# Optimization experiments

Measured on AMD Instinct MI355X. Metric: run time of the kernel, lower is better.

## Reference

```python
import jax, jax.numpy as jnp
import numpy as np

B, C, H, W = 8, 64, 64, 64
DQK = C // 8  # q/k projection dim = 8


def setup_inputs() -> dict:
    key = jax.random.key(0)
    ks = jax.random.split(key, 5)
    return {
        "query": jax.random.normal(ks[0], (B, C, H, W), dtype=jnp.float32),
        "value": jax.random.normal(ks[1], (B, C, H, W), dtype=jnp.float32),
        "Wq": jax.random.normal(ks[2], (DQK, C), dtype=jnp.float32) * (1.0 / np.sqrt(C)),
        "bq": jnp.zeros((DQK,), dtype=jnp.float32),
        "Wk": jax.random.normal(ks[3], (DQK, C), dtype=jnp.float32) * (1.0 / np.sqrt(C)),
        "bk": jnp.zeros((DQK,), dtype=jnp.float32),
        "Wv": jax.random.normal(ks[4], (C, C), dtype=jnp.float32) * (1.0 / np.sqrt(C)),
        "bv": jnp.zeros((C,), dtype=jnp.float32),
    }


def reference(query, value, Wq, bq, Wk, bk, Wv, bv):
    b, c, h, w = value.shape
    n = h * w
    # 1x1 convs are per-pixel matmuls over channels
    q = jnp.einsum("oc,bchw->bohw", Wq, query) + bq[None, :, None, None]
    k = jnp.einsum("oc,bchw->bohw", Wk, query) + bk[None, :, None, None]
    v = jnp.einsum("oc,bchw->bohw", Wv, value) + bv[None, :, None, None]
    proj_q = q.reshape(b, DQK, n).transpose(0, 2, 1)  # [B, N, d]
    proj_k = k.reshape(b, DQK, n)                      # [B, d, N]
    energy = jnp.einsum("bnd,bdm->bnm", proj_q, proj_k)  # [B, N, N]
    attention = jax.nn.softmax(energy, axis=-1)
    proj_v = v.reshape(b, c, n)                        # [B, C, N]
    # out = proj_v @ attention^T
    out = jnp.einsum("bcm,bnm->bcn", proj_v, attention)
    out = out.reshape(b, c, h, w) + value
    return out
```

## Files before the change

### kernel.cpp

```cpp
#include <hip/hip_runtime.h>
#include <hip/hip_bf16.h>

typedef __attribute__((ext_vector_type(8))) __bf16 bf16x8;
typedef __attribute__((ext_vector_type(4))) float f32x4;

#if __has_builtin(__builtin_amdgcn_exp2f)
#define EXP2F(x) __builtin_amdgcn_exp2f(x)
#else
#define EXP2F(x) exp2f(x)
#endif

static constexpr int BB = 8, CC = 64, NN = 4096;
static constexpr size_t QF_OFF = 0;
static constexpr size_t KF_OFF = (size_t)2 << 20;
static constexpr size_t VF_OFF = (size_t)4 << 20;


__global__ __launch_bounds__(512) void proj_kernel(
    const float* __restrict__ query, const float* __restrict__ value,
    const float* __restrict__ Wq, const float* __restrict__ bq,
    const float* __restrict__ Wk, const float* __restrict__ bk,
    const float* __restrict__ Wv, const float* __restrict__ bv,
    char* __restrict__ ws) {
  __shared__ __bf16 vlds[64][72];
  __shared__ float  qlds[64][9];
  __shared__ float  klds[64][9];
  const float LOG2E = 1.4426950408889634f;
  int t = threadIdx.x;
  int part = __builtin_amdgcn_readfirstlane(t >> 6);
  int px = t & 63;
  int blk = blockIdx.x;
  int b = blk >> 6;
  int px0 = (blk & 63) << 6;
  size_t inbase = (size_t)b * CC * NN + px0 + px;

  bool isq = part < 4;
  int qko = (part & 3) * 2;
  const float* __restrict__ Wqk = isq ? Wq : Wk;

  float vacc[8];
  #pragma unroll
  for (int o = 0; o < 8; ++o) vacc[o] = bv[part * 8 + o];
  float qk0 = 0.f, qk1 = 0.f;

  #pragma unroll
  for (int cb = 0; cb < 4; ++cb) {
    float xq[16], xv[16];
    #pragma unroll
    for (int cc = 0; cc < 16; ++cc) {
      int c = cb * 16 + cc;
      xq[cc] = query[inbase + (size_t)c * NN];
      xv[cc] = value[inbase + (size_t)c * NN];
    }
    #pragma unroll
    for (int cc = 0; cc < 16; ++cc) {
      int c = cb * 16 + cc;
      qk0 += Wqk[qko * 64 + c] * xq[cc];
      qk1 += Wqk[(qko + 1) * 64 + c] * xq[cc];
      #pragma unroll
      for (int o = 0; o < 8; ++o) vacc[o] += Wv[(part * 8 + o) * 64 + c] * xv[cc];
    }
  }

  #pragma unroll
  for (int o = 0; o < 8; ++o) vlds[px][part * 8 + o] = (__bf16)vacc[o];
  if (isq) {
    qlds[px][qko]     = (qk0 + bq[qko]) * LOG2E;
    qlds[px][qko + 1] = (qk1 + bq[qko + 1]) * LOG2E;
  } else {
    klds[px][qko]     = qk0 + bk[qko];
    klds[px][qko + 1] = qk1 + bk[qko + 1];
  }
  __syncthreads();

  __bf16* qfrag = (__bf16*)(ws + QF_OFF);
  __bf16* kfrag = (__bf16*)(ws + KF_OFF);
  __bf16* vfrag = (__bf16*)(ws + VF_OFF);
  int l = t & 63, cp = l & 15, qd = l >> 4;

  {
    int jt = t >> 8, ct = (t >> 6) & 3;
    bf16x8 v8;
    #pragma unroll
    for (int r = 0; r < 8; ++r) {
      int jj = (r < 4) ? (4 * qd + r) : (16 + 4 * qd + (r & 3));
      v8[r] = vlds[jt * 32 + jj][ct * 16 + cp];
    }
    int jtg = (blk & 63) * 2 + jt;
    *(bf16x8*)(vfrag + ((((size_t)b * 128 + jtg) * 4 + ct) * 64 + l) * 8) = v8;
  }
  if (t < 256) {
    int jt = t >> 7, th = (t >> 6) & 1;
    int pxl = jt * 32 + th * 16 + (l & 15);
    bf16x8 k8;
    #pragma unroll
    for (int r = 0; r < 8; ++r) {
      float kv = klds[pxl][r];
      __bf16 hi = (__bf16)kv;
      __bf16 lo = (__bf16)(kv - (float)hi);
      k8[r] = (qd < 2) ? hi : lo;
    }
    int jtg = (blk & 63) * 2 + jt;
    *(bf16x8*)(kfrag + ((((size_t)b * 128 + jtg) * 2 + th) * 64 + l) * 8) = k8;
  } else {
    int it = (t >> 6) & 3;
    int il = it * 16 + (l & 15);
    bf16x8 q8;
    #pragma unroll
    for (int r = 0; r < 8; ++r) {
      float qv = qlds[il][r];
      __bf16 hi = (__bf16)qv;
      __bf16 lo = (__bf16)(qv - (float)hi);
      q8[r] = ((qd & 1) == 0) ? hi : lo;
    }
    int itg = (blk & 63) * 4 + it;
    *(bf16x8*)(qfrag + (((size_t)b * 256 + itg) * 64 + l) * 8) = q8;
  }
}

__global__ __launch_bounds__(512, 4) void attn_kernel(
    const char* __restrict__ ws, const float* __restrict__ value,
    float* __restrict__ out) {
  __shared__ float lds_acc[16 * 8 * 64];
  __shared__ float lds_l[4 * 8 * 64];
  const __bf16* qfrag = (const __bf16*)(ws + QF_OFF);
  const __bf16* kfrag = (const __bf16*)(ws + KF_OFF);
  const __bf16* vfrag = (const __bf16*)(ws + VF_OFF);
  int tid = threadIdx.x;
  int w = tid >> 6, lane = tid & 63;
  int blk = blockIdx.x;
  int b = blk >> 6;
  int i0 = (blk & 63) << 6;
  int itg0 = (blk & 63) * 4;

  bf16x8 qf[4];
  #pragma unroll
  for (int it = 0; it < 4; ++it)
    qf[it] = *(const bf16x8*)(qfrag + (((size_t)b * 256 + itg0 + it) * 64 + lane) * 8);

  f32x4 acc[4][4];
  #pragma unroll
  for (int ct = 0; ct < 4; ++ct)
    #pragma unroll
    for (int it = 0; it < 4; ++it) acc[ct][it] = (f32x4){0.f, 0.f, 0.f, 0.f};
  float lsum[4] = {0.f, 0.f, 0.f, 0.f};

  const __bf16* kb = kfrag + (((size_t)b * 128 + w * 16) * 2 * 64 + lane) * 8;
  const __bf16* vb = vfrag + (((size_t)b * 128 + w * 16) * 4 * 64 + lane) * 8;

  for (int itx = 0; itx < 16; ++itx) {
    bf16x8 kf0 = *(const bf16x8*)(kb);
    bf16x8 kf1 = *(const bf16x8*)(kb + 512);
    bf16x8 vf0 = *(const bf16x8*)(vb);
    bf16x8 vf1 = *(const bf16x8*)(vb + 512);
    bf16x8 vf2 = *(const bf16x8*)(vb + 1024);
    bf16x8 vf3 = *(const bf16x8*)(vb + 1536);
    const f32x4 z = (f32x4){0.f, 0.f, 0.f, 0.f};
    #pragma unroll
    for (int it = 0; it < 4; ++it) {
      f32x4 e0 = __builtin_amdgcn_mfma_f32_16x16x32_bf16(kf0, qf[it], z, 0, 0, 0);
      f32x4 e1 = __builtin_amdgcn_mfma_f32_16x16x32_bf16(kf1, qf[it], z, 0, 0, 0);
      bf16x8 pf;
      #pragma unroll
      for (int g = 0; g < 4; ++g) {
        float p0 = EXP2F(e0[g]); lsum[it] += p0; pf[g] = (__bf16)p0;
        float p1 = EXP2F(e1[g]); lsum[it] += p1; pf[4 + g] = (__bf16)p1;
      }
      acc[0][it] = __builtin_amdgcn_mfma_f32_16x16x32_bf16(vf0, pf, acc[0][it], 0, 0, 0);
      acc[1][it] = __builtin_amdgcn_mfma_f32_16x16x32_bf16(vf1, pf, acc[1][it], 0, 0, 0);
      acc[2][it] = __builtin_amdgcn_mfma_f32_16x16x32_bf16(vf2, pf, acc[2][it], 0, 0, 0);
      acc[3][it] = __builtin_amdgcn_mfma_f32_16x16x32_bf16(vf3, pf, acc[3][it], 0, 0, 0);
    }
    kb += 1024;
    vb += 2048;
  }

  #pragma unroll
  for (int it = 0; it < 4; ++it) {
    lsum[it] += __shfl_xor(lsum[it], 16, 64);
    lsum[it] += __shfl_xor(lsum[it], 32, 64);
    lds_l[(it * 8 + w) * 64 + lane] = lsum[it];
  }

  int l = tid & 63;
  #pragma unroll
  for (int p = 0; p < 4; ++p) {
    if (p) __syncthreads();
    #pragma unroll
    for (int ct = 0; ct < 4; ++ct)
      #pragma unroll
      for (int r = 0; r < 4; ++r)
        lds_acc[((ct * 4 + r) * 8 + w) * 64 + lane] = acc[ct][p][r];
    __syncthreads();
    float ls = 0.f;
    #pragma unroll
    for (int ww = 0; ww < 8; ++ww) ls += lds_l[(p * 8 + ww) * 64 + (l & 15)];
    float inv = 1.0f / ls;
    int n = i0 + p * 16 + (l & 15);
    #pragma unroll
    for (int r2 = 0; r2 < 2; ++r2) {
      int e = (tid >> 6) * 2 + r2;
      float s = 0.f;
      #pragma unroll
      for (int ww = 0; ww < 8; ++ww) s += lds_acc[(e * 8 + ww) * 64 + l];
      int c = (e >> 2) * 16 + (l >> 4) * 4 + (e & 3);
      size_t idx = ((size_t)b * CC + c) * NN + n;
      out[idx] = s * inv + value[idx];
    }
  }
}

extern "C" void kernel_launch(void* const* d_in, const int* in_sizes, int n_in,
                              void* d_out, int out_size, void* d_ws, size_t ws_size,
                              hipStream_t stream) {
  const float* query = (const float*)d_in[0];
  const float* value = (const float*)d_in[1];
  const float* Wq = (const float*)d_in[2];
  const float* bq = (const float*)d_in[3];
  const float* Wk = (const float*)d_in[4];
  const float* bk = (const float*)d_in[5];
  const float* Wv = (const float*)d_in[6];
  const float* bv = (const float*)d_in[7];
  float* out = (float*)d_out;

  proj_kernel<<<512, 512, 0, stream>>>(query, value, Wq, bq, Wk, bk, Wv, bv, (char*)d_ws);
  attn_kernel<<<512, 512, 0, stream>>>((const char*)d_ws, value, out);
}
```

Baseline: 126.8 us.

## Switch attention to 32x32x16 MFMA with 128-query tiles and LDS-staged projection

```diff
diff --git a/kernel.cpp b/kernel.cpp
--- a/kernel.cpp
+++ b/kernel.cpp
@@ -2,7 +2,7 @@
 #include <hip/hip_bf16.h>
 
 typedef __attribute__((ext_vector_type(8))) __bf16 bf16x8;
-typedef __attribute__((ext_vector_type(4))) float f32x4;
+typedef __attribute__((ext_vector_type(16))) float f32x16;
 
 #if __has_builtin(__builtin_amdgcn_exp2f)
 #define EXP2F(x) __builtin_amdgcn_exp2f(x)
@@ -22,6 +22,8 @@
     const float* __restrict__ Wk, const float* __restrict__ bk,
     const float* __restrict__ Wv, const float* __restrict__ bv,
     char* __restrict__ ws) {
+  __shared__ float qs[64][64];
+  __shared__ float vvs[64][64];
   __shared__ __bf16 vlds[64][72];
   __shared__ float  qlds[64][9];
   __shared__ float  klds[64][9];
@@ -34,6 +36,14 @@
   int px0 = (blk & 63) << 6;
   size_t inbase = (size_t)b * CC * NN + px0 + px;
 
+  #pragma unroll
+  for (int cc = 0; cc < 8; ++cc) {
+    int c = part * 8 + cc;
+    qs[c][px]  = query[inbase + (size_t)c * NN];
+    vvs[c][px] = value[inbase + (size_t)c * NN];
+  }
+  __syncthreads();
+
   bool isq = part < 4;
   int qko = (part & 3) * 2;
   const float* __restrict__ Wqk = isq ? Wq : Wk;
@@ -48,9 +58,8 @@
     float xq[16], xv[16];
     #pragma unroll
     for (int cc = 0; cc < 16; ++cc) {
-      int c = cb * 16 + cc;
-      xq[cc] = query[inbase + (size_t)c * NN];
-      xv[cc] = value[inbase + (size_t)c * NN];
+      xq[cc] = qs[cb * 16 + cc][px];
+      xv[cc] = vvs[cb * 16 + cc][px];
     }
     #pragma unroll
     for (int cc = 0; cc < 16; ++cc) {
@@ -76,100 +85,114 @@
   __bf16* qfrag = (__bf16*)(ws + QF_OFF);
   __bf16* kfrag = (__bf16*)(ws + KF_OFF);
   __bf16* vfrag = (__bf16*)(ws + VF_OFF);
-  int l = t & 63, cp = l & 15, qd = l >> 4;
+  int l = t & 63, il = l & 31, hA = l >> 5;
+  int w = t >> 6;
 
   {
-    int jt = t >> 8, ct = (t >> 6) & 3;
+    int jt = w >> 2, ct = (w >> 1) & 1, jh = w & 1;
     bf16x8 v8;
     #pragma unroll
     for (int r = 0; r < 8; ++r) {
-      int jj = (r < 4) ? (4 * qd + r) : (16 + 4 * qd + (r & 3));
-      v8[r] = vlds[jt * 32 + jj][ct * 16 + cp];
+      int jj = jt * 32 + jh * 16 + 4 * hA + 8 * (r >> 2) + (r & 3);
+      v8[r] = vlds[jj][ct * 32 + il];
     }
     int jtg = (blk & 63) * 2 + jt;
-    *(bf16x8*)(vfrag + ((((size_t)b * 128 + jtg) * 4 + ct) * 64 + l) * 8) = v8;
-  }
-  if (t < 256) {
-    int jt = t >> 7, th = (t >> 6) & 1;
-    int pxl = jt * 32 + th * 16 + (l & 15);
+    *(bf16x8*)(vfrag + (((((size_t)b * 128 + jtg) * 2 + ct) * 2 + jh) * 64 + l) * 8) = v8;
+  }
+  if (w < 4) {
+    int jt = w >> 1, which = w & 1;
+    int pxl = jt * 32 + il;
     bf16x8 k8;
     #pragma unroll
     for (int r = 0; r < 8; ++r) {
       float kv = klds[pxl][r];
       __bf16 hi = (__bf16)kv;
-      __bf16 lo = (__bf16)(kv - (float)hi);
-      k8[r] = (qd < 2) ? hi : lo;
+      if (which == 0) {
+        k8[r] = hi;
+      } else {
+        __bf16 lo = (__bf16)(kv - (float)hi);
+        k8[r] = (hA == 0) ? lo : (__bf16)0.f;
+      }
     }
     int jtg = (blk & 63) * 2 + jt;
-    *(bf16x8*)(kfrag + ((((size_t)b * 128 + jtg) * 2 + th) * 64 + l) * 8) = k8;
-  } else {
-    int it = (t >> 6) & 3;
-    int il = it * 16 + (l & 15);
+    *(bf16x8*)(kfrag + ((((size_t)b * 128 + jtg) * 2 + which) * 64 + l) * 8) = k8;
+  } else if (w < 6) {
+    int it = w - 4;
+    int pxl = it * 32 + il;
     bf16x8 q8;
     #pragma unroll
     for (int r = 0; r < 8; ++r) {
-      float qv = qlds[il][r];
+      float qv = qlds[pxl][r];
       __bf16 hi = (__bf16)qv;
       __bf16 lo = (__bf16)(qv - (float)hi);
-      q8[r] = ((qd & 1) == 0) ? hi : lo;
-    }
-    int itg = (blk & 63) * 4 + it;
-    *(bf16x8*)(qfrag + (((size_t)b * 256 + itg) * 64 + l) * 8) = q8;
+      q8[r] = (hA == 0) ? hi : lo;
+    }
+    int itg = (blk & 63) * 2 + it;
+    *(bf16x8*)(qfrag + (((size_t)b * 128 + itg) * 64 + l) * 8) = q8;
   }
 }
 
-__global__ __launch_bounds__(512, 4) void attn_kernel(
+__global__ __launch_bounds__(512, 2) void attn_kernel(
     const char* __restrict__ ws, const float* __restrict__ value,
     float* __restrict__ out) {
-  __shared__ float lds_acc[16 * 8 * 64];
-  __shared__ float lds_l[4 * 8 * 64];
+  __shared__ float lds_e[8 * 1028];
+  __shared__ float lsum_lds[32 * 33];
   const __bf16* qfrag = (const __bf16*)(ws + QF_OFF);
   const __bf16* kfrag = (const __bf16*)(ws + KF_OFF);
   const __bf16* vfrag = (const __bf16*)(ws + VF_OFF);
   int tid = threadIdx.x;
   int w = tid >> 6, lane = tid & 63;
   int blk = blockIdx.x;
-  int b = blk >> 6;
-  int i0 = (blk & 63) << 6;
-  int itg0 = (blk & 63) * 4;
+  int b = blk & 7;
+  int ig = blk >> 3;
+  int i0 = ig << 7;
+  int itg0 = ig * 4;
 
   bf16x8 qf[4];
   #pragma unroll
   for (int it = 0; it < 4; ++it)
-    qf[it] = *(const bf16x8*)(qfrag + (((size_t)b * 256 + itg0 + it) * 64 + lane) * 8);
-
-  f32x4 acc[4][4];
-  #pragma unroll
-  for (int ct = 0; ct < 4; ++ct)
-    #pragma unroll
-    for (int it = 0; it < 4; ++it) acc[ct][it] = (f32x4){0.f, 0.f, 0.f, 0.f};
+    qf[it] = *(const bf16x8*)(qfrag + (((size_t)b * 128 + itg0 + it) * 64 + lane) * 8);
+
+  f32x16 acc[4][2];
+  #pragma unroll
+  for (int it = 0; it < 4; ++it)
+    #pragma unroll
+    for (int ct = 0; ct < 2; ++ct)
+      #pragma unroll
+      for (int r = 0; r < 16; ++r) acc[it][ct][r] = 0.f;
   float lsum[4] = {0.f, 0.f, 0.f, 0.f};
 
   const __bf16* kb = kfrag + (((size_t)b * 128 + w * 16) * 2 * 64 + lane) * 8;
   const __bf16* vb = vfrag + (((size_t)b * 128 + w * 16) * 4 * 64 + lane) * 8;
-
-  for (int itx = 0; itx < 16; ++itx) {
-    bf16x8 kf0 = *(const bf16x8*)(kb);
-    bf16x8 kf1 = *(const bf16x8*)(kb + 512);
-    bf16x8 vf0 = *(const bf16x8*)(vb);
-    bf16x8 vf1 = *(const bf16x8*)(vb + 512);
-    bf16x8 vf2 = *(const bf16x8*)(vb + 1024);
-    bf16x8 vf3 = *(const bf16x8*)(vb + 1536);
-    const f32x4 z = (f32x4){0.f, 0.f, 0.f, 0.f};
+  f32x16 Z = {0.f,0.f,0.f,0.f,0.f,0.f,0.f,0.f,0.f,0.f,0.f,0.f,0.f,0.f,0.f,0.f};
+
+  #pragma unroll 1
+  for (int jtl = 0; jtl < 16; ++jtl) {
+    bf16x8 kA1 = *(const bf16x8*)(kb);
+    bf16x8 kA2 = *(const bf16x8*)(kb + 512);
+    bf16x8 vf00 = *(const bf16x8*)(vb);
+    bf16x8 vf01 = *(const bf16x8*)(vb + 512);
+    bf16x8 vf10 = *(const bf16x8*)(vb + 1024);
+    bf16x8 vf11 = *(const bf16x8*)(vb + 1536);
     #pragma unroll
     for (int it = 0; it < 4; ++it) {
-      f32x4 e0 = __builtin_amdgcn_mfma_f32_16x16x32_bf16(kf0, qf[it], z, 0, 0, 0);
-      f32x4 e1 = __builtin_amdgcn_mfma_f32_16x16x32_bf16(kf1, qf[it], z, 0, 0, 0);
-      bf16x8 pf;
-      #pragma unroll
-      for (int g = 0; g < 4; ++g) {
-        float p0 = EXP2F(e0[g]); lsum[it] += p0; pf[g] = (__bf16)p0;
-        float p1 = EXP2F(e1[g]); lsum[it] += p1; pf[4 + g] = (__bf16)p1;
-      }
-      acc[0][it] = __builtin_amdgcn_mfma_f32_16x16x32_bf16(vf0, pf, acc[0][it], 0, 0, 0);
-      acc[1][it] = __builtin_amdgcn_mfma_f32_16x16x32_bf16(vf1, pf, acc[1][it], 0, 0, 0);
-      acc[2][it] = __builtin_amdgcn_mfma_f32_16x16x32_bf16(vf2, pf, acc[2][it], 0, 0, 0);
-      acc[3][it] = __builtin_amdgcn_mfma_f32_16x16x32_bf16(vf3, pf, acc[3][it], 0, 0, 0);
+      f32x16 e = __builtin_amdgcn_mfma_f32_32x32x16_bf16(kA1, qf[it], Z, 0, 0, 0);
+      e = __builtin_amdgcn_mfma_f32_32x32x16_bf16(kA2, qf[it], e, 0, 0, 0);
+      bf16x8 p1, p2;
+      float ls = 0.f;
+      #pragma unroll
+      for (int g = 0; g < 8; ++g) {
+        float p = EXP2F(e[g]);     ls += p; p1[g] = (__bf16)p;
+      }
+      #pragma unroll
+      for (int g = 0; g < 8; ++g) {
+        float p = EXP2F(e[8 + g]); ls += p; p2[g] = (__bf16)p;
+      }
+      lsum[it] += ls;
+      acc[it][0] = __builtin_amdgcn_mfma_f32_32x32x16_bf16(vf00, p1, acc[it][0], 0, 0, 0);
+      acc[it][0] = __builtin_amdgcn_mfma_f32_32x32x16_bf16(vf01, p2, acc[it][0], 0, 0, 0);
+      acc[it][1] = __builtin_amdgcn_mfma_f32_32x32x16_bf16(vf10, p1, acc[it][1], 0, 0, 0);
+      acc[it][1] = __builtin_amdgcn_mfma_f32_32x32x16_bf16(vf11, p2, acc[it][1], 0, 0, 0);
     }
     kb += 1024;
     vb += 2048;
@@ -177,36 +200,53 @@
 
   #pragma unroll
   for (int it = 0; it < 4; ++it) {
-    lsum[it] += __shfl_xor(lsum[it], 16, 64);
     lsum[it] += __shfl_xor(lsum[it], 32, 64);
-    lds_l[(it * 8 + w) * 64 + lane] = lsum[it];
-  }
-
-  int l = tid & 63;
-  #pragma unroll
-  for (int p = 0; p < 4; ++p) {
+    if (lane < 32) lsum_lds[(it * 8 + w) * 33 + lane] = lsum[it];
+  }
+
+  int myi = (2 * tid) & 31;
+  int myc = (2 * tid) >> 5;
+  int src_lane = myi + 32 * ((myc >> 2) & 1);
+  int src_reg  = (myc & 3) + 4 * (myc >> 3);
+  float inv_a[4], inv_b[4];
+
+  #pragma unroll
+  for (int p = 0; p < 8; ++p) {
+    int it = p >> 1, ct = p & 1;
     if (p) __syncthreads();
     #pragma unroll
-    for (int ct = 0; ct < 4; ++ct)
-      #pragma unroll
-      for (int r = 0; r < 4; ++r)
-        lds_acc[((ct * 4 + r) * 8 + w) * 64 + lane] = acc[ct][p][r];
+    for (int r4 = 0; r4 < 4; ++r4) {
+      *(float4*)(lds_e + w * 1028 + lane * 16 + r4 * 4) =
+          (float4){acc[it][ct][r4 * 4], acc[it][ct][r4 * 4 + 1],
+                   acc[it][ct][r4 * 4 + 2], acc[it][ct][r4 * 4 + 3]};
+    }
     __syncthreads();
-    float ls = 0.f;
-    #pragma unroll
-    for (int ww = 0; ww < 8; ++ww) ls += lds_l[(p * 8 + ww) * 64 + (l & 15)];
-    float inv = 1.0f / ls;
-    int n = i0 + p * 16 + (l & 15);
-    #pragma unroll
-    for (int r2 = 0; r2 < 2; ++r2) {
-      int e = (tid >> 6) * 2 + r2;
-      float s = 0.f;
-      #pragma unroll
-      for (int ww = 0; ww < 8; ++ww) s += lds_acc[(e * 8 + ww) * 64 + l];
-      int c = (e >> 2) * 16 + (l >> 4) * 4 + (e & 3);
-      size_t idx = ((size_t)b * CC + c) * NN + n;
-      out[idx] = s * inv + value[idx];
-    }
+    if (p == 0) {
+      #pragma unroll
+      for (int it2 = 0; it2 < 4; ++it2) {
+        float lsA = 0.f, lsB = 0.f;
+        #pragma unroll
+        for (int ww = 0; ww < 8; ++ww) {
+          lsA += lsum_lds[(it2 * 8 + ww) * 33 + myi];
+          lsB += lsum_lds[(it2 * 8 + ww) * 33 + myi + 1];
+        }
+        inv_a[it2] = 1.0f / lsA;
+        inv_b[it2] = 1.0f / lsB;
+      }
+    }
+    float s0 = 0.f, s1 = 0.f;
+    #pragma unroll
+    for (int ww = 0; ww < 8; ++ww) {
+      s0 += lds_e[ww * 1028 + src_lane * 16 + src_reg];
+      s1 += lds_e[ww * 1028 + (src_lane + 1) * 16 + src_reg];
+    }
+    int c = ct * 32 + myc;
+    size_t idx = (((size_t)b * CC + c) * NN) + i0 + it * 32 + myi;
+    float2 vv = *(const float2*)(value + idx);
+    float2 ov;
+    ov.x = s0 * inv_a[it] + vv.x;
+    ov.y = s1 * inv_b[it] + vv.y;
+    *(float2*)(out + idx) = ov;
   }
 }
 
@@ -224,5 +264,5 @@
   float* out = (float*)d_out;
 
   proj_kernel<<<512, 512, 0, stream>>>(query, value, Wq, bq, Wk, bk, Wv, bv, (char*)d_ws);
-  attn_kernel<<<512, 512, 0, stream>>>((const char*)d_ws, value, out);
+  attn_kernel<<<256, 512, 0, stream>>>((const char*)d_ws, value, out);
 }
```

New measurement: 139.8 us. 1.1x slower.
